# Kernel optimization log

Hardware: AMD Instinct MI355X
Metric: run time of the kernel (lower is better)

Reference implementation:

```python
import jax, jax.numpy as jnp
import numpy as np

N = 100_000   # nodes
E = 1_600_000 # edges
F = 128       # input features
H = 128       # hidden
C = 10        # classes
G = 64        # graphs in batch
NUM_LAYERS = 3


def setup_inputs() -> dict:
    key = jax.random.key(0)
    ks = jax.random.split(key, 16)
    x = jax.random.normal(ks[0], (N, F), jnp.float32)
    edge_index = jax.random.randint(ks[1], (2, E), 0, N, dtype=jnp.int64)
    batch = jnp.sort(jax.random.randint(ks[2], (N,), 0, G, dtype=jnp.int64))
    sF = 1.0 / np.sqrt(F)
    sH = 1.0 / np.sqrt(H)
    return {
        "x": x,
        "edge_index": edge_index,
        "batch": batch,
        # conv1 (main) and convs_random_1 branches
        "W1": jax.random.normal(ks[3], (F, H), jnp.float32) * sF,
        "b1": jnp.zeros((H,), jnp.float32),
        "Wr1": jax.random.normal(ks[4], (F, H), jnp.float32) * sF,
        "br1": jnp.zeros((H,), jnp.float32),
        # num_layers-1 hidden GCNConv layers (distinct weights per layer)
        "W2": jax.random.normal(ks[5], (NUM_LAYERS - 1, H, H), jnp.float32) * sH,
        "b2": jnp.zeros((NUM_LAYERS - 1, H), jnp.float32),
        # single shared random-branch conv for all hidden layers
        "Wr": jax.random.normal(ks[6], (H, H), jnp.float32) * sH,
        "br": jnp.zeros((H,), jnp.float32),
        # readout MLP
        "Wl1": jax.random.normal(ks[7], (H, H), jnp.float32) * sH,
        "bl1": jnp.zeros((H,), jnp.float32),
        "Wl2": jax.random.normal(ks[8], (H, C), jnp.float32) * sH,
        "bl2": jnp.zeros((C,), jnp.float32),
    }


def reference(x, edge_index, batch, W1, b1, Wr1, br1, W2, b2, Wr, br,
              Wl1, bl1, Wl2, bl2):
    src, dst = edge_index[0], edge_index[1]
    # GCN symmetric norm with self-loops: deg = in-degree + 1
    deg = jax.ops.segment_sum(jnp.ones((E,), x.dtype), dst, num_segments=N) + 1.0
    dinv_sqrt = deg ** -0.5
    enorm = (dinv_sqrt[src] * dinv_sqrt[dst])[:, None]   # [E,1]
    self_norm = (1.0 / deg)[:, None]                      # [N,1] self-loop coeff

    def gcn_conv(h, W, b):
        h = h @ W                                         # [N,H]
        agg = jax.ops.segment_sum(h[src] * enorm, dst, num_segments=N)
        return agg + h * self_norm + b

    h = jax.nn.relu(0.95 * gcn_conv(x, W1, b1) + 0.05 * gcn_conv(x, Wr1, br1))
    for i in range(NUM_LAYERS - 1):
        h = jax.nn.relu(0.95 * gcn_conv(h, W2[i], b2[i])
                        + 0.05 * gcn_conv(h, Wr, br))

    # global mean pool over graphs
    counts = jax.ops.segment_sum(jnp.ones((N,), x.dtype), batch, num_segments=G)
    pooled = jax.ops.segment_sum(h, batch, num_segments=G) / jnp.maximum(counts, 1.0)[:, None]

    out = jax.nn.relu(pooled @ Wl1 + bl1)
    # dropout p=0.5 is identity in eval mode
    logits = out @ Wl2 + bl2
    return jax.nn.log_softmax(logits, axis=-1)
```

## Files before the change

kernel.cpp:

```cpp
#include <hip/hip_runtime.h>
#include <hip/hip_bf16.h>
#include <hip/hip_fp8.h>

#define NN 100000
#define NE 1600000
#define FF 128
#define HH 128
#define CC 10
#define GG 64

#define NCHUNK 2048
#define CE 782
#define NBUCKET 128
#define BSPAN 782
#define XCONV_BLOCKS 6250
#define PSEG 16

typedef __attribute__((ext_vector_type(8))) short short8;
typedef __attribute__((ext_vector_type(4))) float f32x4;
typedef __attribute__((ext_vector_type(2))) float f32x2;

__device__ inline unsigned short f2bf(float f) {
    union { float f; unsigned int i; } x;
    x.f = f;
    unsigned int r = x.i + 0x7FFF + ((x.i >> 16) & 1);
    return (unsigned short)(r >> 16);
}
__device__ inline unsigned char f8enc(float v) {
    __hip_fp8_e4m3 q(v);
    return (unsigned char)q.__x;
}
__device__ inline float f8dec(unsigned char b) {
    __hip_fp8_e4m3 q;
    q.__x = (__hip_fp8_storage_t)b;
    return (float)q;
}

#if defined(__has_builtin)
#if __has_builtin(__builtin_amdgcn_cvt_pk_f32_fp8)
#define HAVE_CVT_PK_F32_FP8 1
#endif
#endif

__device__ inline void dec8(uint2 v, float* o) {
#ifdef HAVE_CVT_PK_F32_FP8
    f32x2 p;
    p = __builtin_amdgcn_cvt_pk_f32_fp8(v.x, false); o[0] = p[0]; o[1] = p[1];
    p = __builtin_amdgcn_cvt_pk_f32_fp8(v.x, true);  o[2] = p[0]; o[3] = p[1];
    p = __builtin_amdgcn_cvt_pk_f32_fp8(v.y, false); o[4] = p[0]; o[5] = p[1];
    p = __builtin_amdgcn_cvt_pk_f32_fp8(v.y, true);  o[6] = p[0]; o[7] = p[1];
#else
#pragma unroll
    for (int j = 0; j < 4; ++j) {
        o[j]     = f8dec((v.x >> (8 * j)) & 0xFF);
        o[j + 4] = f8dec((v.y >> (8 * j)) & 0xFF);
    }
#endif
}
__device__ inline void dec8p(uint2 v, f32x2* o) {
#ifdef HAVE_CVT_PK_F32_FP8
    o[0] = __builtin_amdgcn_cvt_pk_f32_fp8(v.x, false);
    o[1] = __builtin_amdgcn_cvt_pk_f32_fp8(v.x, true);
    o[2] = __builtin_amdgcn_cvt_pk_f32_fp8(v.y, false);
    o[3] = __builtin_amdgcn_cvt_pk_f32_fp8(v.y, true);
#else
    float d[8]; dec8(v, d);
#pragma unroll
    for (int j = 0; j < 4; ++j) { o[j][0] = d[2 * j]; o[j][1] = d[2 * j + 1]; }
#endif
}
__device__ inline uint2 enc8(const float* d) {
    unsigned a = 0, b = 0;
#pragma unroll
    for (int j = 0; j < 4; ++j) {
        a |= ((unsigned)f8enc(d[j])) << (8 * j);
        b |= ((unsigned)f8enc(d[j + 4])) << (8 * j);
    }
    uint2 o; o.x = a; o.y = b; return o;
}

__global__ __launch_bounds__(256) void combo_kernel(const float* __restrict__ x,
                                                    unsigned char* __restrict__ x8,
                                                    const float* __restrict__ W1, const float* __restrict__ b1,
                                                    const float* __restrict__ Wr1, const float* __restrict__ br1,
                                                    const float* __restrict__ W2, const float* __restrict__ b2,
                                                    const float* __restrict__ Wr, const float* __restrict__ br,
                                                    unsigned short* __restrict__ Wpack, float* __restrict__ bc) {
    int bid = blockIdx.x;
    if (bid < XCONV_BLOCKS) {
        int i = bid * 256 + threadIdx.x;
        float4 v0 = ((const float4*)x)[i * 2];
        float4 v1 = ((const float4*)x)[i * 2 + 1];
        float d[8] = {v0.x, v0.y, v0.z, v0.w, v1.x, v1.y, v1.z, v1.w};
        ((uint2*)x8)[i] = enc8(d);
        return;
    }
    int idx = (bid - XCONV_BLOCKS) * 256 + threadIdx.x;
    int l = idx / 16384, rem = idx % 16384;
    int cb = rem / 2048;
    int kb = (rem / 512) % 4;
    int lane = (rem / 8) % 64;
    int j = rem % 8;
    int k = kb * 32 + (lane >> 4) * 8 + j;
    int c = cb * 16 + (lane & 15);
    int wi = k * HH + c;
    float v = (l == 0) ? 0.95f * W1[wi] + 0.05f * Wr1[wi]
                       : 0.95f * W2[(l - 1) * 16384 + wi] + 0.05f * Wr[wi];
    Wpack[idx] = f2bf(v);
    if (rem < HH) {
        bc[l * HH + rem] = (l == 0) ? 0.95f * b1[rem] + 0.05f * br1[rem]
                                    : 0.95f * b2[(l - 1) * HH + rem] + 0.05f * br[rem];
    }
}

__global__ __launch_bounds__(256) void partA1_kernel(const int* __restrict__ ei,
                                                     int* __restrict__ cc) {
    __shared__ int h[NBUCKET];
    int c = blockIdx.x, t = threadIdx.x;
    if (t < NBUCKET) h[t] = 0;
    __syncthreads();
    int beg = c * CE, end = min(beg + CE, NE);
    for (int e = beg + t; e < end; e += 256)
        atomicAdd(&h[ei[NE + e] / BSPAN], 1);
    __syncthreads();
    if (t < NBUCKET) cc[c * NBUCKET + t] = h[t];
}

__global__ __launch_bounds__(256) void partA2_kernel(int* __restrict__ cc,
                                                     int* __restrict__ tot) {
    __shared__ int sh[256];
    int b = blockIdx.x, t = threadIdx.x;
    int v[8]; int s = 0;
#pragma unroll
    for (int i = 0; i < 8; ++i) { v[i] = cc[(t * 8 + i) * NBUCKET + b]; s += v[i]; }
    sh[t] = s; __syncthreads();
    for (int off = 1; off < 256; off <<= 1) {
        int x = (t >= off) ? sh[t - off] : 0; __syncthreads();
        sh[t] += x; __syncthreads();
    }
    int excl = sh[t] - s;
#pragma unroll
    for (int i = 0; i < 8; ++i) {
        cc[(t * 8 + i) * NBUCKET + b] = excl;
        excl += v[i];
    }
    if (t == 255) tot[b] = sh[255];
}

__global__ __launch_bounds__(256) void partA3_kernel(const int* __restrict__ ei,
                                                     const int* __restrict__ cc,
                                                     const int* __restrict__ tot,
                                                     uint2* __restrict__ eb) {
    __shared__ int stot[NBUCKET];
    __shared__ int cur[NBUCKET];
    int c = blockIdx.x, t = threadIdx.x;
    if (t < NBUCKET) stot[t] = tot[t];
    __syncthreads();
    for (int off = 1; off < NBUCKET; off <<= 1) {
        int x = (t < NBUCKET && t >= off) ? stot[t - off] : 0;
        __syncthreads();
        if (t < NBUCKET) stot[t] += x;
        __syncthreads();
    }
    if (t < NBUCKET) cur[t] = (stot[t] - tot[t]) + cc[c * NBUCKET + t];
    __syncthreads();
    int beg = c * CE, end = min(beg + CE, NE);
    for (int e = beg + t; e < end; e += 256) {
        int d = ei[NE + e];
        int s = ei[e];
        int p = atomicAdd(&cur[d / BSPAN], 1);
        uint2 pr; pr.x = (unsigned)d; pr.y = (unsigned)s;
        eb[p] = pr;
    }
}

__global__ __launch_bounds__(256) void partB1_kernel(const uint2* __restrict__ eb,
                                                     const int* __restrict__ tot,
                                                     int* __restrict__ offs,
                                                     float* __restrict__ dinv) {
    __shared__ int hcnt[BSPAN];
    __shared__ int sh[256];
    __shared__ int gbase_sh;
    int b = blockIdx.x, t = threadIdx.x;
    int lo = b * BSPAN;
    int span = min(BSPAN, NN - lo);
    if (span <= 0) return;
    for (int i = t; i < span; i += 256) hcnt[i] = 0;
    if (t == 0) {
        int g = 0;
        for (int i = 0; i < b; ++i) g += tot[i];
        gbase_sh = g;
    }
    __syncthreads();
    int gbase = gbase_sh;
    int len = tot[b];
    const uint2* ebb = eb + (size_t)gbase;
    for (int e = t; e < len; e += 256)
        atomicAdd(&hcnt[(int)ebb[e].x - lo], 1);
    __syncthreads();
    int base = t * 4;
    int v[4]; int s = 0;
#pragma unroll
    for (int j = 0; j < 4; ++j) { int i = base + j; v[j] = (i < span) ? hcnt[i] : 0; s += v[j]; }
    sh[t] = s; __syncthreads();
    for (int off = 1; off < 256; off <<= 1) {
        int x = (t >= off) ? sh[t - off] : 0; __syncthreads();
        sh[t] += x; __syncthreads();
    }
    int excl = sh[t] - s + gbase;
#pragma unroll
    for (int j = 0; j < 4; ++j) {
        int i = base + j;
        if (i < span) {
            offs[lo + i] = excl;
            dinv[lo + i] = rsqrtf((float)v[j] + 1.0f);
            excl += v[j];
        }
    }
    if (b == NBUCKET - 1 && t == 0) offs[NN] = NE;
}

__global__ __launch_bounds__(256) void partB2_kernel(const uint2* __restrict__ eb,
                                                     const int* __restrict__ offs,
                                                     int* __restrict__ csrc) {
    __shared__ int lcur[BSPAN];
    int b = blockIdx.x, t = threadIdx.x;
    int lo = b * BSPAN;
    int span = min(BSPAN, NN - lo);
    if (span <= 0) return;
    for (int i = t; i < span; i += 256) lcur[i] = offs[lo + i];
    __syncthreads();
    int ebeg = offs[lo];
    int eend = offs[min(lo + span, NN)];
    for (int e = ebeg + t; e < eend; e += 256) {
        uint2 pr = eb[e];
        int p = atomicAdd(&lcur[(int)pr.x - lo], 1);
        csrc[p] = (int)pr.y;
    }
}

__global__ __launch_bounds__(256) void gemm_mfma_kernel(const unsigned char* __restrict__ A8,
                                                        const unsigned short* __restrict__ Wp,
                                                        const float* __restrict__ dinv,
                                                        unsigned char* __restrict__ out8,
                                                        int nrows) {
    __shared__ unsigned char f8s[64][128];
    int w = threadIdx.x >> 6;
    int l = threadIdx.x & 63;
    int m0 = blockIdx.x * 64 + w * 16;
    int kg = l >> 4;
    int cl = l & 15;
    int arow = m0 + cl;

    short8 a[4];
    if (arow < nrows) {
        const uint2* Ar = (const uint2*)(A8 + (size_t)arow * HH);
#pragma unroll
        for (int kb = 0; kb < 4; ++kb) {
            uint2 v = Ar[kb * 4 + kg];
            float d[8]; dec8(v, d);
            short8 t;
#pragma unroll
            for (int j = 0; j < 8; ++j) t[j] = (short)f2bf(d[j]);
            a[kb] = t;
        }
    } else {
        short8 z = {};
#pragma unroll
        for (int kb = 0; kb < 4; ++kb) a[kb] = z;
    }

    float dv[4];
#pragma unroll
    for (int r = 0; r < 4; ++r) {
        int orow = m0 + kg * 4 + r;
        dv[r] = (orow < nrows) ? dinv[orow] : 0.f;
    }

#pragma unroll
    for (int cb = 0; cb < 8; ++cb) {
        f32x4 acc = {0.f, 0.f, 0.f, 0.f};
#pragma unroll
        for (int kb = 0; kb < 4; ++kb) {
            short8 b = *(const short8*)(Wp + (size_t)(cb * 4 + kb) * 512 + l * 8);
            acc = __builtin_amdgcn_mfma_f32_16x16x32_bf16(a[kb], b, acc, 0, 0, 0);
        }
#pragma unroll
        for (int r = 0; r < 4; ++r)
            f8s[w * 16 + kg * 4 + r][cb * 16 + cl] = f8enc(acc[r] * dv[r]);
    }
    __syncthreads();
    int blk0 = blockIdx.x * 64;
    for (int u = threadIdx.x; u < 512; u += 256) {
        int row = u >> 3, c16 = u & 7;
        int grow = blk0 + row;
        if (grow < nrows)
            ((uint4*)out8)[(size_t)grow * 8 + c16] = ((const uint4*)&f8s[row][0])[c16];
    }
}

__global__ __launch_bounds__(256) void agg_relu_kernel(const unsigned char* __restrict__ t8,
                                                       const int* __restrict__ offs,
                                                       const int* __restrict__ csrc,
                                                       const float* __restrict__ dinv,
                                                       const float* __restrict__ bias,
                                                       unsigned char* __restrict__ hOut) {
    int n = blockIdx.x * 16 + (threadIdx.x >> 4);
    if (n >= NN) return;
    int lane = threadIdx.x & 15;
    int beg = offs[n], end = offs[n + 1];
    const uint2* g8 = (const uint2*)t8;
    f32x2 acc2[4] = {};
    f32x2 d2[4];
    int e = beg;
    for (; e + 3 < end; e += 4) {
        int s0 = csrc[e], s1 = csrc[e + 1], s2 = csrc[e + 2], s3 = csrc[e + 3];
        uint2 v0 = g8[(size_t)s0 * 16 + lane];
        uint2 v1 = g8[(size_t)s1 * 16 + lane];
        uint2 v2 = g8[(size_t)s2 * 16 + lane];
        uint2 v3 = g8[(size_t)s3 * 16 + lane];
        dec8p(v0, d2);
#pragma unroll
        for (int k = 0; k < 4; ++k) acc2[k] += d2[k];
        dec8p(v1, d2);
#pragma unroll
        for (int k = 0; k < 4; ++k) acc2[k] += d2[k];
        dec8p(v2, d2);
#pragma unroll
        for (int k = 0; k < 4; ++k) acc2[k] += d2[k];
        dec8p(v3, d2);
#pragma unroll
        for (int k = 0; k < 4; ++k) acc2[k] += d2[k];
    }
    for (; e < end; ++e) {
        uint2 v = g8[(size_t)csrc[e] * 16 + lane];
        dec8p(v, d2);
#pragma unroll
        for (int k = 0; k < 4; ++k) acc2[k] += d2[k];
    }
    {
        uint2 v = g8[(size_t)n * 16 + lane];
        dec8p(v, d2);
#pragma unroll
        for (int k = 0; k < 4; ++k) acc2[k] += d2[k];
    }
    float dn = dinv[n];
    float4 bv0 = ((const float4*)bias)[lane * 2];
    float4 bv1 = ((const float4*)bias)[lane * 2 + 1];
    float bb[8] = {bv0.x, bv0.y, bv0.z, bv0.w, bv1.x, bv1.y, bv1.z, bv1.w};
    float o[8];
#pragma unroll
    for (int j = 0; j < 8; ++j)
        o[j] = fmaxf(fmaf(acc2[j >> 1][j & 1], dn, bb[j]), 0.f);
    ((uint2*)hOut)[(size_t)n * 16 + lane] = enc8(o);
}

__global__ __launch_bounds__(256) void poolseg_kernel(const unsigned char* __restrict__ h8,
                                                      const int* __restrict__ batch,
                                                      float* __restrict__ psum_seg) {
    int g = blockIdx.x >> 4;
    int seg = blockIdx.x & (PSEG - 1);
    int t = threadIdx.x;
    int lo = 0, hi = NN;
    while (lo < hi) { int m = (lo + hi) >> 1; if (batch[m] < g) lo = m + 1; else hi = m; }
    int lb = lo;
    lo = 0; hi = NN;
    while (lo < hi) { int m = (lo + hi) >> 1; if (batch[m] <= g) lo = m + 1; else hi = m; }
    int ub = lo;
    int len = ub - lb;
    int b0 = lb + (int)(((long long)len * seg) / PSEG);
    int b1 = lb + (int)(((long long)len * (seg + 1)) / PSEG);

    int fg = t & 15;
    int rg = t >> 4;
    const uint2* gp = (const uint2*)h8;
    f32x2 acc2[4] = {};
    f32x2 d2[4];
    for (int n = b0 + rg; n < b1; n += 16) {
        uint2 v = gp[(size_t)n * 16 + fg];
        dec8p(v, d2);
#pragma unroll
        for (int k = 0; k < 4; ++k) acc2[k] += d2[k];
    }
    __shared__ float red[256][8];
#pragma unroll
    for (int j = 0; j < 8; ++j) red[t][j] = acc2[j >> 1][j & 1];
    __syncthreads();
    for (int off = 8; off >= 1; off >>= 1) {
        if (rg < off) {
#pragma unroll
            for (int j = 0; j < 8; ++j) red[t][j] += red[t + off * 16][j];
        }
        __syncthreads();
    }
    if (t < 16) {
#pragma unroll
        for (int j = 0; j < 8; ++j)
            psum_seg[((size_t)g * PSEG + seg) * HH + t * 8 + j] = red[t][j];
    }
}

__global__ __launch_bounds__(128) void mlp2_kernel(const float* __restrict__ psum_seg,
                                                   const int* __restrict__ batch,
                                                   const float* __restrict__ Wl1,
                                                   const float* __restrict__ bl1,
                                                   const float* __restrict__ Wl2,
                                                   const float* __restrict__ bl2,
                                                   float* __restrict__ out) {
    __shared__ float p[128], o1[128], lg[CC];
    int g = blockIdx.x, t = threadIdx.x;
    int lo = 0, hi = NN;
    while (lo < hi) { int m = (lo + hi) >> 1; if (batch[m] < g) lo = m + 1; else hi = m; }
    int lb = lo;
    lo = 0; hi = NN;
    while (lo < hi) { int m = (lo + hi) >> 1; if (batch[m] <= g) lo = m + 1; else hi = m; }
    int len = lo - lb;
    float a = 0.f;
#pragma unroll
    for (int s = 0; s < PSEG; ++s)
        a += psum_seg[((size_t)g * PSEG + s) * HH + t];
    p[t] = a / fmaxf((float)len, 1.f);
    __syncthreads();
    float acc = bl1[t];
    for (int k = 0; k < HH; ++k) acc = fmaf(p[k], Wl1[k * HH + t], acc);
    o1[t] = fmaxf(acc, 0.f);
    __syncthreads();
    if (t < CC) {
        float a2 = bl2[t];
        for (int j = 0; j < HH; ++j) a2 = fmaf(o1[j], Wl2[j * CC + t], a2);
        lg[t] = a2;
    }
    __syncthreads();
    if (t == 0) {
        float m = lg[0];
        for (int c = 1; c < CC; ++c) m = fmaxf(m, lg[c]);
        float s = 0.f;
        for (int c = 0; c < CC; ++c) s += expf(lg[c] - m);
        float ls = logf(s);
        for (int c = 0; c < CC; ++c) out[g * CC + c] = lg[c] - m - ls;
    }
}

extern "C" void kernel_launch(void* const* d_in, const int* in_sizes, int n_in,
                              void* d_out, int out_size, void* d_ws, size_t ws_size,
                              hipStream_t stream) {
    const float* x   = (const float*)d_in[0];
    const int*   ei  = (const int*)d_in[1];
    const int*   bat = (const int*)d_in[2];
    const float* W1  = (const float*)d_in[3];
    const float* b1  = (const float*)d_in[4];
    const float* Wr1 = (const float*)d_in[5];
    const float* br1 = (const float*)d_in[6];
    const float* W2  = (const float*)d_in[7];
    const float* b2  = (const float*)d_in[8];
    const float* Wr  = (const float*)d_in[9];
    const float* br  = (const float*)d_in[10];
    const float* Wl1 = (const float*)d_in[11];
    const float* bl1 = (const float*)d_in[12];
    const float* Wl2 = (const float*)d_in[13];
    const float* bl2 = (const float*)d_in[14];
    float* out = (float*)d_out;

    char* base = (char*)d_ws;
    size_t off = 0;
    auto alloc = [&](size_t bytes) {
        void* p = base + off;
        off += (bytes + 255) & ~(size_t)255;
        return p;
    };
    unsigned char* x8   = (unsigned char*)alloc((size_t)NN * HH);
    unsigned char* h8   = (unsigned char*)alloc((size_t)NN * HH);
    unsigned char* t8   = (unsigned char*)alloc((size_t)NN * HH);
    uint2* eb     = (uint2*)alloc((size_t)NE * 8);
    int*   cc     = (int*)alloc((size_t)NCHUNK * NBUCKET * 4);
    int*   csrc   = (int*)alloc((size_t)NE * 4);
    int*   offs   = (int*)alloc((size_t)(NN + 1) * 4);
    float* dinv   = (float*)alloc((size_t)NN * 4);
    int*   tot    = (int*)alloc(NBUCKET * 4);
    unsigned short* Wpack = (unsigned short*)alloc(3 * 16384 * 2);
    float* bc     = (float*)alloc(3 * HH * 4);
    float* psum_seg = (float*)alloc((size_t)GG * PSEG * HH * 4);
    (void)ws_size; (void)in_sizes; (void)n_in; (void)out_size;

    combo_kernel<<<XCONV_BLOCKS + 192, 256, 0, stream>>>(x, x8, W1, b1, Wr1, br1,
                                                         W2, b2, Wr, br, Wpack, bc);

    partA1_kernel<<<NCHUNK, 256, 0, stream>>>(ei, cc);
    partA2_kernel<<<NBUCKET, 256, 0, stream>>>(cc, tot);
    partA3_kernel<<<NCHUNK, 256, 0, stream>>>(ei, cc, tot, eb);
    partB1_kernel<<<NBUCKET, 256, 0, stream>>>(eb, tot, offs, dinv);
    partB2_kernel<<<NBUCKET, 256, 0, stream>>>(eb, offs, csrc);

    const int GEMM_BLOCKS = (NN + 63) / 64;
    const int AGG_BLOCKS = (NN + 15) / 16;
    gemm_mfma_kernel<<<GEMM_BLOCKS, 256, 0, stream>>>(x8, Wpack, dinv, t8, NN);
    agg_relu_kernel<<<AGG_BLOCKS, 256, 0, stream>>>(t8, offs, csrc, dinv, bc, h8);
    gemm_mfma_kernel<<<GEMM_BLOCKS, 256, 0, stream>>>(h8, Wpack + 16384, dinv, t8, NN);
    agg_relu_kernel<<<AGG_BLOCKS, 256, 0, stream>>>(t8, offs, csrc, dinv, bc + HH, h8);
    gemm_mfma_kernel<<<GEMM_BLOCKS, 256, 0, stream>>>(h8, Wpack + 2 * 16384, dinv, t8, NN);
    agg_relu_kernel<<<AGG_BLOCKS, 256, 0, stream>>>(t8, offs, csrc, dinv, bc + 2 * HH, h8);

    poolseg_kernel<<<GG * PSEG, 256, 0, stream>>>(h8, bat, psum_seg);
    mlp2_kernel<<<GG, 128, 0, stream>>>(psum_seg, bat, Wl1, bl1, Wl2, bl2, out);
}
```

Measured before the change: 253.2 us.

## Pack edge buckets to 32-bit, fuse CSR build, widen aggregation loads, hardware fp8 encode

Edge bucket entries are packed into one 32-bit word holding the source id and the local destination offset, which halves the intermediate buffer traffic. The two CSR-build kernels are merged so the scatter reuses the in-shared-memory prefix sums and saves a launch. The aggregation kernel now uses 8 lanes per node with 16-byte loads instead of 16 lanes with 8-byte loads, and folds the self-loop into the tail loop. FP8 encoding switches to the packed hardware conversion builtin when available; its rounding may differ slightly from the software path.

```diff
diff --git a/kernel.cpp b/kernel.cpp
--- a/kernel.cpp
+++ b/kernel.cpp
@@ -15,6 +15,7 @@
 #define BSPAN 782
 #define XCONV_BLOCKS 6250
 #define PSEG 16
+#define SRCBITS 17
 
 typedef __attribute__((ext_vector_type(8))) short short8;
 typedef __attribute__((ext_vector_type(4))) float f32x4;
@@ -26,7 +27,7 @@
     unsigned int r = x.i + 0x7FFF + ((x.i >> 16) & 1);
     return (unsigned short)(r >> 16);
 }
-__device__ inline unsigned char f8enc(float v) {
+__device__ inline unsigned char f8enc_sw(float v) {
     __hip_fp8_e4m3 q(v);
     return (unsigned char)q.__x;
 }
@@ -39,6 +40,9 @@
 #if defined(__has_builtin)
 #if __has_builtin(__builtin_amdgcn_cvt_pk_f32_fp8)
 #define HAVE_CVT_PK_F32_FP8 1
+#endif
+#if __has_builtin(__builtin_amdgcn_cvt_pk_fp8_f32)
+#define HAVE_CVT_PK_FP8 1
 #endif
 #endif
 
@@ -69,14 +73,28 @@
     for (int j = 0; j < 4; ++j) { o[j][0] = d[2 * j]; o[j][1] = d[2 * j + 1]; }
 #endif
 }
+__device__ inline unsigned enc_pk4(float a, float b, float c, float d) {
+#ifdef HAVE_CVT_PK_FP8
+    int w = __builtin_amdgcn_cvt_pk_fp8_f32(a, b, 0, false);
+    w = __builtin_amdgcn_cvt_pk_fp8_f32(c, d, w, true);
+    return (unsigned)w;
+#else
+    return (unsigned)f8enc_sw(a) | ((unsigned)f8enc_sw(b) << 8) |
+           ((unsigned)f8enc_sw(c) << 16) | ((unsigned)f8enc_sw(d) << 24);
+#endif
+}
+__device__ inline unsigned char f8enc1(float v) {
+#ifdef HAVE_CVT_PK_FP8
+    return (unsigned char)(__builtin_amdgcn_cvt_pk_fp8_f32(v, v, 0, false) & 0xFF);
+#else
+    return f8enc_sw(v);
+#endif
+}
 __device__ inline uint2 enc8(const float* d) {
-    unsigned a = 0, b = 0;
-#pragma unroll
-    for (int j = 0; j < 4; ++j) {
-        a |= ((unsigned)f8enc(d[j])) << (8 * j);
-        b |= ((unsigned)f8enc(d[j + 4])) << (8 * j);
-    }
-    uint2 o; o.x = a; o.y = b; return o;
+    uint2 o;
+    o.x = enc_pk4(d[0], d[1], d[2], d[3]);
+    o.y = enc_pk4(d[4], d[5], d[6], d[7]);
+    return o;
 }
 
 __global__ __launch_bounds__(256) void combo_kernel(const float* __restrict__ x,
@@ -150,7 +168,7 @@
 __global__ __launch_bounds__(256) void partA3_kernel(const int* __restrict__ ei,
                                                      const int* __restrict__ cc,
                                                      const int* __restrict__ tot,
-                                                     uint2* __restrict__ eb) {
+                                                     unsigned* __restrict__ eb32) {
     __shared__ int stot[NBUCKET];
     __shared__ int cur[NBUCKET];
     int c = blockIdx.x, t = threadIdx.x;
@@ -168,17 +186,20 @@
     for (int e = beg + t; e < end; e += 256) {
         int d = ei[NE + e];
         int s = ei[e];
-        int p = atomicAdd(&cur[d / BSPAN], 1);
-        uint2 pr; pr.x = (unsigned)d; pr.y = (unsigned)s;
-        eb[p] = pr;
-    }
-}
-
-__global__ __launch_bounds__(256) void partB1_kernel(const uint2* __restrict__ eb,
-                                                     const int* __restrict__ tot,
-                                                     int* __restrict__ offs,
-                                                     float* __restrict__ dinv) {
+        int b = d / BSPAN;
+        int ld = d - b * BSPAN;
+        int p = atomicAdd(&cur[b], 1);
+        eb32[p] = (unsigned)s | ((unsigned)ld << SRCBITS);
+    }
+}
+
+__global__ __launch_bounds__(256) void partB_kernel(const unsigned* __restrict__ eb32,
+                                                    const int* __restrict__ tot,
+                                                    int* __restrict__ offs,
+                                                    float* __restrict__ dinv,
+                                                    int* __restrict__ csrc) {
     __shared__ int hcnt[BSPAN];
+    __shared__ int lcur[BSPAN];
     __shared__ int sh[256];
     __shared__ int gbase_sh;
     int b = blockIdx.x, t = threadIdx.x;
@@ -194,9 +215,9 @@
     __syncthreads();
     int gbase = gbase_sh;
     int len = tot[b];
-    const uint2* ebb = eb + (size_t)gbase;
+    const unsigned* ebb = eb32 + (size_t)gbase;
     for (int e = t; e < len; e += 256)
-        atomicAdd(&hcnt[(int)ebb[e].x - lo], 1);
+        atomicAdd(&hcnt[ebb[e] >> SRCBITS], 1);
     __syncthreads();
     int base = t * 4;
     int v[4]; int s = 0;
@@ -213,29 +234,17 @@
         int i = base + j;
         if (i < span) {
             offs[lo + i] = excl;
+            lcur[i] = excl;
             dinv[lo + i] = rsqrtf((float)v[j] + 1.0f);
             excl += v[j];
         }
     }
     if (b == NBUCKET - 1 && t == 0) offs[NN] = NE;
-}
-
-__global__ __launch_bounds__(256) void partB2_kernel(const uint2* __restrict__ eb,
-                                                     const int* __restrict__ offs,
-                                                     int* __restrict__ csrc) {
-    __shared__ int lcur[BSPAN];
-    int b = blockIdx.x, t = threadIdx.x;
-    int lo = b * BSPAN;
-    int span = min(BSPAN, NN - lo);
-    if (span <= 0) return;
-    for (int i = t; i < span; i += 256) lcur[i] = offs[lo + i];
-    __syncthreads();
-    int ebeg = offs[lo];
-    int eend = offs[min(lo + span, NN)];
-    for (int e = ebeg + t; e < eend; e += 256) {
-        uint2 pr = eb[e];
-        int p = atomicAdd(&lcur[(int)pr.x - lo], 1);
-        csrc[p] = (int)pr.y;
+    __syncthreads();
+    for (int e = t; e < len; e += 256) {
+        unsigned pr = ebb[e];
+        int p = atomicAdd(&lcur[pr >> SRCBITS], 1);
+        csrc[p] = (int)(pr & ((1u << SRCBITS) - 1));
     }
 }
 
@@ -287,7 +296,7 @@
         }
 #pragma unroll
         for (int r = 0; r < 4; ++r)
-            f8s[w * 16 + kg * 4 + r][cb * 16 + cl] = f8enc(acc[r] * dv[r]);
+            f8s[w * 16 + kg * 4 + r][cb * 16 + cl] = f8enc1(acc[r] * dv[r]);
     }
     __syncthreads();
     int blk0 = blockIdx.x * 64;
@@ -305,54 +314,80 @@
                                                        const float* __restrict__ dinv,
                                                        const float* __restrict__ bias,
                                                        unsigned char* __restrict__ hOut) {
-    int n = blockIdx.x * 16 + (threadIdx.x >> 4);
+    int n = blockIdx.x * 32 + (threadIdx.x >> 3);
     if (n >= NN) return;
-    int lane = threadIdx.x & 15;
+    int lane = threadIdx.x & 7;
     int beg = offs[n], end = offs[n + 1];
-    const uint2* g8 = (const uint2*)t8;
-    f32x2 acc2[4] = {};
+    const uint4* g16 = (const uint4*)t8;
+    f32x2 acc2[8] = {};
     f32x2 d2[4];
     int e = beg;
     for (; e + 3 < end; e += 4) {
         int s0 = csrc[e], s1 = csrc[e + 1], s2 = csrc[e + 2], s3 = csrc[e + 3];
-        uint2 v0 = g8[(size_t)s0 * 16 + lane];
-        uint2 v1 = g8[(size_t)s1 * 16 + lane];
-        uint2 v2 = g8[(size_t)s2 * 16 + lane];
-        uint2 v3 = g8[(size_t)s3 * 16 + lane];
-        dec8p(v0, d2);
+        uint4 v0 = g16[(size_t)s0 * 8 + lane];
+        uint4 v1 = g16[(size_t)s1 * 8 + lane];
+        uint4 v2 = g16[(size_t)s2 * 8 + lane];
+        uint4 v3 = g16[(size_t)s3 * 8 + lane];
+        uint2 a, b;
+        a.x = v0.x; a.y = v0.y; b.x = v0.z; b.y = v0.w;
+        dec8p(a, d2);
 #pragma unroll
         for (int k = 0; k < 4; ++k) acc2[k] += d2[k];
-        dec8p(v1, d2);
+        dec8p(b, d2);
+#pragma unroll
+        for (int k = 0; k < 4; ++k) acc2[k + 4] += d2[k];
+        a.x = v1.x; a.y = v1.y; b.x = v1.z; b.y = v1.w;
+        dec8p(a, d2);
 #pragma unroll
         for (int k = 0; k < 4; ++k) acc2[k] += d2[k];
-        dec8p(v2, d2);
+        dec8p(b, d2);
+#pragma unroll
+        for (int k = 0; k < 4; ++k) acc2[k + 4] += d2[k];
+        a.x = v2.x; a.y = v2.y; b.x = v2.z; b.y = v2.w;
+        dec8p(a, d2);
 #pragma unroll
         for (int k = 0; k < 4; ++k) acc2[k] += d2[k];
-        dec8p(v3, d2);
+        dec8p(b, d2);
+#pragma unroll
+        for (int k = 0; k < 4; ++k) acc2[k + 4] += d2[k];
+        a.x = v3.x; a.y = v3.y; b.x = v3.z; b.y = v3.w;
+        dec8p(a, d2);
 #pragma unroll
         for (int k = 0; k < 4; ++k) acc2[k] += d2[k];
-    }
-    for (; e < end; ++e) {
-        uint2 v = g8[(size_t)csrc[e] * 16 + lane];
-        dec8p(v, d2);
+        dec8p(b, d2);
+#pragma unroll
+        for (int k = 0; k < 4; ++k) acc2[k + 4] += d2[k];
+    }
+    for (; e <= end; ++e) {
+        int s = (e < end) ? csrc[e] : n;
+        uint4 v = g16[(size_t)s * 8 + lane];
+        uint2 a, b;
+        a.x = v.x; a.y = v.y; b.x = v.z; b.y = v.w;
+        dec8p(a, d2);
 #pragma unroll
         for (int k = 0; k < 4; ++k) acc2[k] += d2[k];
-    }
-    {
-        uint2 v = g8[(size_t)n * 16 + lane];
-        dec8p(v, d2);
-#pragma unroll
-        for (int k = 0; k < 4; ++k) acc2[k] += d2[k];
+        dec8p(b, d2);
+#pragma unroll
+        for (int k = 0; k < 4; ++k) acc2[k + 4] += d2[k];
     }
     float dn = dinv[n];
-    float4 bv0 = ((const float4*)bias)[lane * 2];
-    float4 bv1 = ((const float4*)bias)[lane * 2 + 1];
-    float bb[8] = {bv0.x, bv0.y, bv0.z, bv0.w, bv1.x, bv1.y, bv1.z, bv1.w};
-    float o[8];
-#pragma unroll
-    for (int j = 0; j < 8; ++j)
+    const float4* bv = (const float4*)(bias + lane * 16);
+    float bb[16];
+    float4 b0 = bv[0], b1 = bv[1], b2 = bv[2], b3 = bv[3];
+    bb[0]=b0.x; bb[1]=b0.y; bb[2]=b0.z; bb[3]=b0.w;
+    bb[4]=b1.x; bb[5]=b1.y; bb[6]=b1.z; bb[7]=b1.w;
+    bb[8]=b2.x; bb[9]=b2.y; bb[10]=b2.z; bb[11]=b2.w;
+    bb[12]=b3.x; bb[13]=b3.y; bb[14]=b3.z; bb[15]=b3.w;
+    float o[16];
+#pragma unroll
+    for (int j = 0; j < 16; ++j)
         o[j] = fmaxf(fmaf(acc2[j >> 1][j & 1], dn, bb[j]), 0.f);
-    ((uint2*)hOut)[(size_t)n * 16 + lane] = enc8(o);
+    uint4 w;
+    w.x = enc_pk4(o[0], o[1], o[2], o[3]);
+    w.y = enc_pk4(o[4], o[5], o[6], o[7]);
+    w.z = enc_pk4(o[8], o[9], o[10], o[11]);
+    w.w = enc_pk4(o[12], o[13], o[14], o[15]);
+    ((uint4*)hOut)[(size_t)n * 8 + lane] = w;
 }
 
 __global__ __launch_bounds__(256) void poolseg_kernel(const unsigned char* __restrict__ h8,
@@ -471,7 +506,7 @@
     unsigned char* x8   = (unsigned char*)alloc((size_t)NN * HH);
     unsigned char* h8   = (unsigned char*)alloc((size_t)NN * HH);
     unsigned char* t8   = (unsigned char*)alloc((size_t)NN * HH);
-    uint2* eb     = (uint2*)alloc((size_t)NE * 8);
+    unsigned* eb32 = (unsigned*)alloc((size_t)NE * 4);
     int*   cc     = (int*)alloc((size_t)NCHUNK * NBUCKET * 4);
     int*   csrc   = (int*)alloc((size_t)NE * 4);
     int*   offs   = (int*)alloc((size_t)(NN + 1) * 4);
@@ -487,12 +522,11 @@
 
     partA1_kernel<<<NCHUNK, 256, 0, stream>>>(ei, cc);
     partA2_kernel<<<NBUCKET, 256, 0, stream>>>(cc, tot);
-    partA3_kernel<<<NCHUNK, 256, 0, stream>>>(ei, cc, tot, eb);
-    partB1_kernel<<<NBUCKET, 256, 0, stream>>>(eb, tot, offs, dinv);
-    partB2_kernel<<<NBUCKET, 256, 0, stream>>>(eb, offs, csrc);
+    partA3_kernel<<<NCHUNK, 256, 0, stream>>>(ei, cc, tot, eb32);
+    partB_kernel<<<NBUCKET, 256, 0, stream>>>(eb32, tot, offs, dinv, csrc);
 
     const int GEMM_BLOCKS = (NN + 63) / 64;
-    const int AGG_BLOCKS = (NN + 15) / 16;
+    const int AGG_BLOCKS = (NN + 31) / 32;
     gemm_mfma_kernel<<<GEMM_BLOCKS, 256, 0, stream>>>(x8, Wpack, dinv, t8, NN);
     agg_relu_kernel<<<AGG_BLOCKS, 256, 0, stream>>>(t8, offs, csrc, dinv, bc, h8);
     gemm_mfma_kernel<<<GEMM_BLOCKS, 256, 0, stream>>>(h8, Wpack + 16384, dinv, t8, NN);
```

Result: faster. 247.7 us (-2.2%).
